# Optimization experiments

Measured on AMD Instinct MI355X. Metric: run time of the kernel, lower is better.

The kernel has to match this reference:

```python
import jax, jax.numpy as jnp
import numpy as np

B, S = 1, 2048
HID, NH, NKV, HD = 2048, 16, 4, 128
NREP = NH // NKV  # 4
WIN = 1024
ROPE_THETA = 10000.0


def rotate_half(t):
    t1, t2 = jnp.split(t, 2, axis=-1)
    return jnp.concatenate([-t2, t1], axis=-1)


def setup_inputs() -> dict:
    key = jax.random.key(0)
    ks = jax.random.split(key, 5)
    x = jax.random.normal(ks[0], (B, S, HID), dtype=jnp.float32)
    # causal sliding-window additive mask: 0 where attended, -1e9 elsewhere
    i = jnp.arange(S)
    allowed = (i[None, :] <= i[:, None]) & (i[:, None] - i[None, :] < WIN)
    attention_mask = jnp.where(allowed, 0.0, -1e9).astype(jnp.float32)[None, None]  # [1,1,S,S]
    wq = jax.random.normal(ks[1], (NH * HD, HID), dtype=jnp.float32) * 0.02
    wk = jax.random.normal(ks[2], (NKV * HD, HID), dtype=jnp.float32) * 0.02
    wv = jax.random.normal(ks[3], (NKV * HD, HID), dtype=jnp.float32) * 0.02
    wo = jax.random.normal(ks[4], (HID, NH * HD), dtype=jnp.float32) * 0.02
    return {"x": x, "attention_mask": attention_mask, "wq": wq, "wk": wk, "wv": wv, "wo": wo}


def reference(x, attention_mask, wq, wk, wv, wo):
    b, s, _ = x.shape
    q = (x @ wq.T).reshape(b, s, NH, HD)
    k = (x @ wk.T).reshape(b, s, NKV, HD)
    v = (x @ wv.T).reshape(b, s, NKV, HD)
    # rotary embeddings (HF-style rotate_half)
    inv_freq = 1.0 / (ROPE_THETA ** (jnp.arange(0, HD, 2, dtype=jnp.float32) / HD))
    freqs = jnp.arange(s, dtype=jnp.float32)[:, None] * inv_freq[None, :]  # [s, HD/2]
    emb = jnp.concatenate([freqs, freqs], axis=-1)  # [s, HD]
    cos = jnp.cos(emb)[None, :, None, :]
    sin = jnp.sin(emb)[None, :, None, :]
    q = q * cos + rotate_half(q) * sin
    k = k * cos + rotate_half(k) * sin
    # GQA: repeat kv heads
    k = jnp.repeat(k, NREP, axis=2)  # [b, s, NH, HD]
    v = jnp.repeat(v, NREP, axis=2)
    scores = jnp.einsum('bqhd,bkhd->bhqk', q, k) / jnp.sqrt(jnp.float32(HD)) + attention_mask
    probs = jax.nn.softmax(scores.astype(jnp.float32), axis=-1).astype(q.dtype)
    out = jnp.einsum('bhqk,bkhd->bqhd', probs, v).reshape(b, s, NH * HD)
    return out @ wo.T
```

## Files before the change

kernel.cpp:

```cpp
#include <hip/hip_runtime.h>


#define AS1 __attribute__((address_space(1)))
#define AS3 __attribute__((address_space(3)))

typedef short v8s __attribute__((ext_vector_type(8)));
typedef short v4s __attribute__((ext_vector_type(4)));
typedef float v4f __attribute__((ext_vector_type(4)));

__device__ __forceinline__ void gload16(const void* g, void* l) {
  __builtin_amdgcn_global_load_lds((AS1 void*)g, (AS3 void*)l, 16, 0, 0);
}

__device__ __forceinline__ short f2bf(float f) {
  union { float f; unsigned u; } v; v.f = f;
  unsigned r = (v.u + 0x7FFFu + ((v.u >> 16) & 1u)) >> 16;
  return (short)r;
}
__device__ __forceinline__ short f2bf_hu(float f) {
  union { float f; unsigned u; } v; v.f = f;
  return (short)((v.u + 0x8000u) >> 16);
}
__device__ __forceinline__ float bf2f(short h) {
  union { unsigned u; float f; } v; v.u = ((unsigned)(unsigned short)h) << 16;
  return v.f;
}
__device__ __forceinline__ bool sniff_bf16(const unsigned* mask) {
  return mask[1] == 0xCE6ECE6Eu;
}

__device__ __forceinline__ int colmap(int w, int nt, int r) {
  return (w & 1) * 32 + (nt & 1) * 16 + (nt >> 1) * 64 + r;
}

#define ROPE_L2T (13.287712379549449f / 64.0f)
#define Q_SCALE  (1.4426950408889634f * 0.08838834764831845f)
#define SM_SHIFT 8.0f

template <bool BF> struct Raw8;
template <> struct Raw8<true>  { v8s v; };
template <> struct Raw8<false> { float4 a, b; };

template <bool BF> __device__ __forceinline__ Raw8<BF> ldraw(const void* p, size_t e);
template <> __device__ __forceinline__ Raw8<true> ldraw<true>(const void* p, size_t e) {
  Raw8<true> r; r.v = *(const v8s*)((const short*)p + e); return r;
}
template <> __device__ __forceinline__ Raw8<false> ldraw<false>(const void* p, size_t e) {
  Raw8<false> r; const float* f = (const float*)p + e;
  r.a = *(const float4*)f; r.b = *(const float4*)(f + 4); return r;
}
template <bool BF> __device__ __forceinline__ v8s cvt8(const Raw8<BF>& r);
template <> __device__ __forceinline__ v8s cvt8<true>(const Raw8<true>& r) { return r.v; }
template <> __device__ __forceinline__ v8s cvt8<false>(const Raw8<false>& r) {
  v8s o;
  o[0] = f2bf(r.a.x); o[1] = f2bf(r.a.y); o[2] = f2bf(r.a.z); o[3] = f2bf(r.a.w);
  o[4] = f2bf(r.b.x); o[5] = f2bf(r.b.y); o[6] = f2bf(r.b.z); o[7] = f2bf(r.b.w);
  return o;
}

__global__ __launch_bounds__(256) void convert_kernel(
    const void* __restrict__ X, const void* __restrict__ WQ,
    const void* __restrict__ WK, const void* __restrict__ WV,
    const void* __restrict__ WO, const unsigned* __restrict__ mask,
    short* __restrict__ Xbf, short* __restrict__ Wqkvbf, short* __restrict__ WObf)
{
  const bool bf = sniff_bf16(mask);
  size_t e = ((size_t)blockIdx.x * 256 + threadIdx.x) * 8;
  const void* src; short* dst; size_t off, doff;
  if (e < 4194304)       { src = X;  dst = Xbf;  off = e; doff = e; }
  else if (e < 10485760) {
    size_t wv = e - 4194304; dst = Wqkvbf; doff = wv;
    if (wv < 4194304)      { src = WQ; off = wv; }
    else if (wv < 5242880) { src = WK; off = wv - 4194304; }
    else                   { src = WV; off = wv - 5242880; }
  }
  else                   { src = WO; dst = WObf; off = e - 10485760; doff = off; }
  v8s v = bf ? ldraw<true>(src, off).v : cvt8<false>(ldraw<false>(src, off));
  *(v8s*)&dst[doff] = v;
}

#define MM(I, J) acc##I##J = __builtin_amdgcn_mfma_f32_16x16x32_bf16(a##I, b##J, acc##I##J, 0, 0, 0)

#define GEMM128_BODY(Aptr, Bptr) \
  const int tid = threadIdx.x; \
  const int w = tid >> 6, lane = tid & 63; \
  const int quad = lane >> 4, r = lane & 15; \
  const int wm = (w >> 1) * 64; \
  const int rlo = lane >> 2, c8 = (lane & 3) * 8; \
  size_t ga[4]; short* la[4]; size_t gb[4]; short* lb[4]; \
  _Pragma("unroll") for (int j = 0; j < 4; ++j) { \
    int cc = w * 4 + j; int p = cc >> 3, local = cc & 7; \
    ga[j] = (size_t)(m0 + local * 16 + rlo) * 2048 + p * 32 + c8; \
    la[j] = lA + cc * 512; \
    gb[j] = (size_t)(n0 + local * 16 + rlo) * 2048 + p * 32 + c8; \
    lb[j] = lB + cc * 512; } \
  v4f acc00 = v4f{0.f, 0.f, 0.f, 0.f}; \
  v4f acc01 = acc00, acc02 = acc00, acc03 = acc00; \
  v4f acc10 = acc00, acc11 = acc00, acc12 = acc00, acc13 = acc00; \
  v4f acc20 = acc00, acc21 = acc00, acc22 = acc00, acc23 = acc00; \
  v4f acc30 = acc00, acc31 = acc00, acc32 = acc00, acc33 = acc00; \
  for (int k0 = 0; k0 < 2048; k0 += 64) { \
    if (k0) __syncthreads(); \
    _Pragma("unroll") for (int j = 0; j < 4; ++j) gload16(Aptr + ga[j] + k0, la[j]); \
    _Pragma("unroll") for (int j = 0; j < 4; ++j) gload16(Bptr + gb[j] + k0, lb[j]); \
    __syncthreads(); \
    _Pragma("unroll") for (int ks = 0; ks < 2; ++ks) { \
      const int ab = ks * 4096; \
      v8s a0 = *(const v8s*)&lA[ab + (wm +  0 + r) * 32 + quad * 8]; \
      v8s a1 = *(const v8s*)&lA[ab + (wm + 16 + r) * 32 + quad * 8]; \
      v8s a2 = *(const v8s*)&lA[ab + (wm + 32 + r) * 32 + quad * 8]; \
      v8s a3 = *(const v8s*)&lA[ab + (wm + 48 + r) * 32 + quad * 8]; \
      v8s b0 = *(const v8s*)&lB[ab + colmap(w, 0, r) * 32 + quad * 8]; \
      v8s b1 = *(const v8s*)&lB[ab + colmap(w, 1, r) * 32 + quad * 8]; \
      v8s b2 = *(const v8s*)&lB[ab + colmap(w, 2, r) * 32 + quad * 8]; \
      v8s b3 = *(const v8s*)&lB[ab + colmap(w, 3, r) * 32 + quad * 8]; \
      MM(0,0); MM(0,1); MM(0,2); MM(0,3); \
      MM(1,0); MM(1,1); MM(1,2); MM(1,3); \
      MM(2,0); MM(2,1); MM(2,2); MM(2,3); \
      MM(3,0); MM(3,1); MM(3,2); MM(3,3); \
    } \
  }

__global__ __launch_bounds__(256, 2) void gemm_qkv_dma(
    const short* __restrict__ Xbf, const short* __restrict__ Wqkvbf,
    short* __restrict__ Qo, short* __restrict__ Ko, short* __restrict__ VTo)
{
  __shared__ __align__(16) short lA[128 * 64];
  __shared__ __align__(16) short lB[128 * 64];
  const int m0 = blockIdx.x * 128;
  const int n0 = blockIdx.y * 128;
  GEMM128_BODY(Xbf, Wqkvbf)

  const int rowb = m0 + wm + quad * 4;
  if (n0 < 2560) {
    const bool isQ = (n0 < 2048);
    short* dst = isQ ? Qo : Ko;
    const int ld = isQ ? 2048 : 512;
    const int base = isQ ? n0 : (n0 - 2048);
    const float sc = isQ ? Q_SCALE : 1.0f;
#define ROPE_ST(MT, NT, X1, X2) { \
      int d = (w & 1) * 32 + NT * 16 + r; \
      float inv = exp2f(-(float)d * ROPE_L2T); \
      _Pragma("unroll") for (int i = 0; i < 4; ++i) { \
        int row = rowb + MT * 16 + i; \
        float ang = (float)row * inv; \
        float cs = cosf(ang), sn = sinf(ang); \
        float x1 = X1[i], x2 = X2[i]; \
        dst[(size_t)row * ld + base + d]      = f2bf((x1 * cs - x2 * sn) * sc); \
        dst[(size_t)row * ld + base + d + 64] = f2bf((x2 * cs + x1 * sn) * sc); } }
    ROPE_ST(0, 0, acc00, acc02) ROPE_ST(0, 1, acc01, acc03)
    ROPE_ST(1, 0, acc10, acc12) ROPE_ST(1, 1, acc11, acc13)
    ROPE_ST(2, 0, acc20, acc22) ROPE_ST(2, 1, acc21, acc23)
    ROPE_ST(3, 0, acc30, acc32) ROPE_ST(3, 1, acc31, acc33)
#undef ROPE_ST
  } else {
#define VT_ST(MT, NT, A) { \
      int row = rowb + MT * 16; \
      int vcol = n0 - 2560 + colmap(w, NT, r); \
      v4s pk; \
      _Pragma("unroll") for (int i = 0; i < 4; ++i) pk[i] = f2bf(A[i]); \
      *(v4s*)&VTo[(size_t)vcol * 2048 + row] = pk; }
    VT_ST(0, 0, acc00) VT_ST(0, 1, acc01) VT_ST(0, 2, acc02) VT_ST(0, 3, acc03)
    VT_ST(1, 0, acc10) VT_ST(1, 1, acc11) VT_ST(1, 2, acc12) VT_ST(1, 3, acc13)
    VT_ST(2, 0, acc20) VT_ST(2, 1, acc21) VT_ST(2, 2, acc22) VT_ST(2, 3, acc23)
    VT_ST(3, 0, acc30) VT_ST(3, 1, acc31) VT_ST(3, 2, acc32) VT_ST(3, 3, acc33)
#undef VT_ST
  }
}

__global__ __launch_bounds__(256, 2) void gemm_out_dma(
    const short* __restrict__ A, const short* __restrict__ WObf,
    const unsigned* __restrict__ mask, void* __restrict__ Out)
{
  __shared__ __align__(16) short lA[128 * 64];
  __shared__ __align__(16) short lB[128 * 64];
  const int m0 = blockIdx.x * 128;
  const int n0 = blockIdx.y * 128;
  GEMM128_BODY(A, WObf)

  const bool bf = sniff_bf16(mask);
  const int rowb = m0 + wm + quad * 4;
#define OUT_ST(MT, NT, ACC) { \
    int row = rowb + MT * 16; \
    int col = n0 + colmap(w, NT, r); \
    _Pragma("unroll") for (int i = 0; i < 4; ++i) { \
      size_t idx = (size_t)(row + i) * 2048 + col; \
      if (bf) ((short*)Out)[idx] = f2bf(ACC[i]); \
      else    ((float*)Out)[idx] = ACC[i]; } }
  OUT_ST(0, 0, acc00) OUT_ST(0, 1, acc01) OUT_ST(0, 2, acc02) OUT_ST(0, 3, acc03)
  OUT_ST(1, 0, acc10) OUT_ST(1, 1, acc11) OUT_ST(1, 2, acc12) OUT_ST(1, 3, acc13)
  OUT_ST(2, 0, acc20) OUT_ST(2, 1, acc21) OUT_ST(2, 2, acc22) OUT_ST(2, 3, acc23)
  OUT_ST(3, 0, acc30) OUT_ST(3, 1, acc31) OUT_ST(3, 2, acc32) OUT_ST(3, 3, acc33)
#undef OUT_ST
}

template <bool BFA, bool BFB>
__device__ __forceinline__ void gemm64x128_loop(
    const void* __restrict__ A, const void* __restrict__ Bt,
    int m0, int brow0, short* lA, short* lB, v4f acc[2][4])
{
  const int tid = threadIdx.x;
  const int w = tid >> 6, lane = tid & 63;
  const int quad = lane >> 4, r = lane & 15;
  const int wm = (w >> 1) * 32;

  int uoffA[2]; size_t ea[2];
#pragma unroll
  for (int j = 0; j < 2; ++j) {
    int u = tid + 256 * j;
    int row = u >> 3, c = (u & 7) * 8;
    uoffA[j] = (c & 32) * 64 + row * 32 + (c & 31);
    ea[j] = (size_t)(m0 + row) * 2048 + c;
  }
  int uoffB[4]; size_t eb[4];
#pragma unroll
  for (int j = 0; j < 4; ++j) {
    int u = tid + 256 * j;
    int row = u >> 3, c = (u & 7) * 8;
    uoffB[j] = (c & 32) * 128 + row * 32 + (c & 31);
    eb[j] = (size_t)(brow0 + row) * 2048 + c;
  }

  for (int k0 = 0; k0 < 2048; k0 += 64) {
    Raw8<BFA> ta[2]; Raw8<BFB> tb[4];
#pragma unroll
    for (int j = 0; j < 2; ++j) ta[j] = ldraw<BFA>(A, ea[j] + k0);
#pragma unroll
    for (int j = 0; j < 4; ++j) tb[j] = ldraw<BFB>(Bt, eb[j] + k0);
    if (k0) __syncthreads();
#pragma unroll
    for (int j = 0; j < 2; ++j) *(v8s*)&lA[uoffA[j]] = cvt8<BFA>(ta[j]);
#pragma unroll
    for (int j = 0; j < 4; ++j) *(v8s*)&lB[uoffB[j]] = cvt8<BFB>(tb[j]);
    __syncthreads();
#pragma unroll
    for (int ks = 0; ks < 2; ++ks) {
      v8s a[2], b[4];
#pragma unroll
      for (int mt = 0; mt < 2; ++mt)
        a[mt] = *(const v8s*)&lA[ks * 2048 + (wm + mt * 16 + r) * 32 + quad * 8];
#pragma unroll
      for (int nt = 0; nt < 4; ++nt)
        b[nt] = *(const v8s*)&lB[ks * 4096 + colmap(w, nt, r) * 32 + quad * 8];
#pragma unroll
      for (int mt = 0; mt < 2; ++mt)
#pragma unroll
        for (int nt = 0; nt < 4; ++nt)
          acc[mt][nt] = __builtin_amdgcn_mfma_f32_16x16x32_bf16(a[mt], b[nt], acc[mt][nt], 0, 0, 0);
    }
  }
}

__device__ __forceinline__ void qkv_epilogue_fb(
    v4f acc[2][4], int m0, int n0, short* Qo, short* Ko, short* VTo)
{
  const int tid = threadIdx.x;
  const int w = tid >> 6, lane = tid & 63;
  const int quad = lane >> 4, r = lane & 15;
  const int wm = (w >> 1) * 32;
  const int rowb = m0 + wm + quad * 4;

  if (n0 < 2560) {
    const bool isQ = (n0 < 2048);
    short* dst = isQ ? Qo : Ko;
    const int ld = isQ ? 2048 : 512;
    const int base = isQ ? n0 : (n0 - 2048);
    const float sc = isQ ? Q_SCALE : 1.0f;
#pragma unroll
    for (int nt = 0; nt < 2; ++nt) {
      int d = (w & 1) * 32 + nt * 16 + r;
      float inv = exp2f(-(float)d * ROPE_L2T);
#pragma unroll
      for (int mt = 0; mt < 2; ++mt)
#pragma unroll
        for (int i = 0; i < 4; ++i) {
          int row = rowb + mt * 16 + i;
          float ang = (float)row * inv;
          float cs = cosf(ang), sn = sinf(ang);
          float x1 = acc[mt][nt][i], x2 = acc[mt][nt + 2][i];
          dst[(size_t)row * ld + base + d]      = f2bf((x1 * cs - x2 * sn) * sc);
          dst[(size_t)row * ld + base + d + 64] = f2bf((x2 * cs + x1 * sn) * sc);
        }
    }
  } else {
#pragma unroll
    for (int mt = 0; mt < 2; ++mt)
#pragma unroll
      for (int nt = 0; nt < 4; ++nt) {
        int row = rowb + mt * 16;
        int vcol = n0 - 2560 + colmap(w, nt, r);
        v4s pk;
#pragma unroll
        for (int i = 0; i < 4; ++i) pk[i] = f2bf(acc[mt][nt][i]);
        *(v4s*)&VTo[(size_t)vcol * 2048 + row] = pk;
      }
  }
}

__global__ __launch_bounds__(256, 3) void gemm_qkv_fb(
    const void* __restrict__ X, const void* __restrict__ WQ,
    const void* __restrict__ WK, const void* __restrict__ WV,
    const unsigned* __restrict__ mask,
    short* __restrict__ Qo, short* __restrict__ Ko, short* __restrict__ VTo)
{
  __shared__ __align__(16) short lA[64 * 64];
  __shared__ __align__(16) short lB[128 * 64];
  const int m0 = blockIdx.x * 64;
  const int n0 = blockIdx.y * 128;
  const void* Bt; int brow0;
  if (n0 < 2048)      { Bt = WQ; brow0 = n0; }
  else if (n0 < 2560) { Bt = WK; brow0 = n0 - 2048; }
  else                { Bt = WV; brow0 = n0 - 2560; }

  v4f acc[2][4];
#pragma unroll
  for (int i = 0; i < 2; ++i)
#pragma unroll
    for (int j = 0; j < 4; ++j) acc[i][j] = v4f{0.f, 0.f, 0.f, 0.f};

  if (sniff_bf16(mask)) gemm64x128_loop<true, true>(X, Bt, m0, brow0, lA, lB, acc);
  else                  gemm64x128_loop<false, false>(X, Bt, m0, brow0, lA, lB, acc);
  qkv_epilogue_fb(acc, m0, n0, Qo, Ko, VTo);
}

__global__ __launch_bounds__(256, 3) void gemm_out_fb(
    const short* __restrict__ A, const void* __restrict__ WO,
    const unsigned* __restrict__ mask, void* __restrict__ Out)
{
  __shared__ __align__(16) short lA[64 * 64];
  __shared__ __align__(16) short lB[128 * 64];
  const bool bf = sniff_bf16(mask);
  const int m0 = blockIdx.x * 64;
  const int n0 = blockIdx.y * 128;

  v4f acc[2][4];
#pragma unroll
  for (int i = 0; i < 2; ++i)
#pragma unroll
    for (int j = 0; j < 4; ++j) acc[i][j] = v4f{0.f, 0.f, 0.f, 0.f};

  if (bf) gemm64x128_loop<true, true>(A, WO, m0, n0, lA, lB, acc);
  else    gemm64x128_loop<true, false>(A, WO, m0, n0, lA, lB, acc);

  const int tid = threadIdx.x;
  const int w = tid >> 6, lane = tid & 63;
  const int quad = lane >> 4, r = lane & 15;
  const int wm = (w >> 1) * 32;
  const int rowb = m0 + wm + quad * 4;
#pragma unroll
  for (int mt = 0; mt < 2; ++mt)
#pragma unroll
    for (int nt = 0; nt < 4; ++nt) {
      int row = rowb + mt * 16;
      int col = n0 + colmap(w, nt, r);
#pragma unroll
      for (int i = 0; i < 4; ++i) {
        size_t idx = (size_t)(row + i) * 2048 + col;
        if (bf) ((short*)Out)[idx] = f2bf(acc[mt][nt][i]);
        else    ((float*)Out)[idx] = acc[mt][nt][i];
      }
    }
}

__global__ __launch_bounds__(256, 1) void attn_kernel(
    const short* __restrict__ Q, const short* __restrict__ Kb,
    const short* __restrict__ VT, short* __restrict__ Ao)
{
  __shared__ __align__(16) short lK[64 * 128];
  __shared__ __align__(16) short lV[128 * 64];
  __shared__ __align__(16) short lP[4][16 * 72];

  const int bx = blockIdx.x;
  const int qb = bx >> 4, h = bx & 15;
  const int hk = h >> 2;
  const int q0 = qb * 64;
  const int tid = threadIdx.x, w = tid >> 6, lane = tid & 63;
  const int quad = lane >> 4, r = lane & 15;
  const int wq0 = q0 + w * 16;
  short* lPw = lP[w];

  v8s qa[4];
#pragma unroll
  for (int ks = 0; ks < 4; ++ks)
    qa[ks] = *(const v8s*)(Q + (size_t)(wq0 + r) * 2048 + h * 128 + ks * 32 + quad * 8);

  v8s ones;
#pragma unroll
  for (int j = 0; j < 8; ++j) ones[j] = (short)0x3F80;

  v4f Oa[8];
#pragma unroll
  for (int dt = 0; dt < 8; ++dt) Oa[dt] = v4f{0.f, 0.f, 0.f, 0.f};
  v4f La = v4f{0.f, 0.f, 0.f, 0.f};

  const int t0 = (q0 >= 1024) ? ((q0 - 1023) >> 6) : 0;
  const int t1 = qb;

  for (int t = t0; t <= t1; ++t) {
    const int key0 = t << 6;
    v8s tK[4], tV[4];
#pragma unroll
    for (int u = 0; u < 4; ++u) {
      int lin = (w * 4 + u) * 64 + lane;
      int krow = lin >> 4, kcc = lin & 15;
      tK[u] = *(const v8s*)(Kb + (size_t)(key0 + krow) * 512 + hk * 128 + ((kcc ^ krow) & 15) * 8);
      int vrow = lin >> 3, vcc = lin & 7;
      tV[u] = *(const v8s*)(VT + (size_t)(hk * 128 + vrow) * 2048 + key0 + ((vcc ^ vrow) & 7) * 8);
    }
    if (t > t0) __syncthreads();
#pragma unroll
    for (int u = 0; u < 4; ++u) {
      int lin = (w * 4 + u) * 64 + lane;
      *(v8s*)&lK[lin * 8] = tK[u];
      *(v8s*)&lV[lin * 8] = tV[u];
    }
    __syncthreads();

    v4f s4[4];
#pragma unroll
    for (int nt = 0; nt < 4; ++nt) s4[nt] = v4f{0.f, 0.f, 0.f, 0.f};
    __builtin_amdgcn_s_setprio(1);
#pragma unroll
    for (int ks = 0; ks < 4; ++ks)
#pragma unroll
      for (int nt = 0; nt < 4; ++nt) {
        v8s bk = *(const v8s*)&lK[(nt * 16 + r) * 128 + (((ks * 4 + quad) ^ r) & 15) * 8];
        s4[nt] = __builtin_amdgcn_mfma_f32_16x16x32_bf16(qa[ks], bk, s4[nt], 0, 0, 0);
      }
    __builtin_amdgcn_s_setprio(0);

    const bool full = (key0 + 63 <= wq0) && (wq0 + 15 - key0 < 1024);

    if (full) {
#pragma unroll
      for (int nt = 0; nt < 4; ++nt)
#pragma unroll
        for (int i = 0; i < 4; ++i)
          lPw[(quad * 4 + i) * 72 + nt * 16 + r] = f2bf_hu(exp2f(s4[nt][i] - SM_SHIFT));
    } else {
#pragma unroll
      for (int nt = 0; nt < 4; ++nt) {
        int d0 = wq0 + quad * 4 - key0 - nt * 16 - r;
#pragma unroll
        for (int i = 0; i < 4; ++i) {
          bool ok = (unsigned)(d0 + i) < 1024u;
          lPw[(quad * 4 + i) * 72 + nt * 16 + r] =
              ok ? f2bf_hu(exp2f(s4[nt][i] - SM_SHIFT)) : (short)0;
        }
      }
    }

    __builtin_amdgcn_s_setprio(1);
#pragma unroll
    for (int ks2 = 0; ks2 < 2; ++ks2) {
      v8s ap = *(const v8s*)&lPw[r * 72 + ks2 * 32 + quad * 8];
      La = __builtin_amdgcn_mfma_f32_16x16x32_bf16(ap, ones, La, 0, 0, 0);
#pragma unroll
      for (int dt = 0; dt < 8; ++dt) {
        v8s bv = *(const v8s*)&lV[(dt * 16 + r) * 64 + (((ks2 * 4 + quad) ^ r) & 7) * 8];
        Oa[dt] = __builtin_amdgcn_mfma_f32_16x16x32_bf16(ap, bv, Oa[dt], 0, 0, 0);
      }
    }
    __builtin_amdgcn_s_setprio(0);
  }

  float invl[4];
#pragma unroll
  for (int i = 0; i < 4; ++i) invl[i] = (La[i] > 0.f) ? 1.0f / La[i] : 0.f;
#pragma unroll
  for (int dt = 0; dt < 8; ++dt)
#pragma unroll
    for (int i = 0; i < 4; ++i) {
      int q = wq0 + quad * 4 + i;
      Ao[(size_t)q * 2048 + h * 128 + dt * 16 + r] = f2bf(Oa[dt][i] * invl[i]);
    }
}

extern "C" void kernel_launch(void* const* d_in, const int* in_sizes, int n_in,
                              void* d_out, int out_size, void* d_ws, size_t ws_size,
                              hipStream_t stream) {
  const void*     x    = d_in[0];
  const unsigned* mask = (const unsigned*)d_in[1];
  const void*     wq   = d_in[2];
  const void*     wk   = d_in[3];
  const void*     wv   = d_in[4];
  const void*     wo   = d_in[5];

  short* Q  = (short*)d_out;
  short* Kb = (short*)d_ws;
  short* VT = Kb + (size_t)1048576;
  short* Ao = VT + (size_t)1048576;

  const size_t NEED = 41943040ull;
  if (ws_size >= NEED) {
    short* Xbf    = Ao + (size_t)4194304;
    short* Wqkvbf = Xbf + (size_t)4194304;
    short* WObf   = Wqkvbf + (size_t)6291456;
    convert_kernel<<<7168, 256, 0, stream>>>(x, wq, wk, wv, wo, mask, Xbf, Wqkvbf, WObf);
    gemm_qkv_dma<<<dim3(16, 24), 256, 0, stream>>>(Xbf, Wqkvbf, Q, Kb, VT);
    attn_kernel<<<512, 256, 0, stream>>>(Q, Kb, VT, Ao);
    gemm_out_dma<<<dim3(16, 16), 256, 0, stream>>>(Ao, WObf, mask, d_out);
  } else {
    gemm_qkv_fb<<<dim3(32, 24), 256, 0, stream>>>(x, wq, wk, wv, mask, Q, Kb, VT);
    attn_kernel<<<512, 256, 0, stream>>>(Q, Kb, VT, Ao);
    gemm_out_fb<<<dim3(32, 16), 256, 0, stream>>>(Ao, wo, mask, d_out);
  }
}
```

Measured before the change: 235.3 us.

## Double-buffer LDS tiles in QKV and output projection GEMMs

Replaces the single-buffered K loop in both projection GEMMs with a double-buffered pipeline. The next 64-wide K tile is DMA-loaded into the alternate LDS buffer while the current tile is computed, using vmcnt waits and raw s_barrier instead of two __syncthreads per step. This is meant to hide global-load latency behind MFMA work. It doubles LDS per block to 64KB, which may limit occupancy to fewer blocks per CU.

```diff
diff --git a/kernel.cpp b/kernel.cpp
--- a/kernel.cpp
+++ b/kernel.cpp
@@ -81,55 +81,72 @@
 
 #define MM(I, J) acc##I##J = __builtin_amdgcn_mfma_f32_16x16x32_bf16(a##I, b##J, acc##I##J, 0, 0, 0)
 
-#define GEMM128_BODY(Aptr, Bptr) \
+#define STAGE8(Aptr, Bptr, K0, DA, DB) \
+    _Pragma("unroll") for (int j = 0; j < 4; ++j) gload16(Aptr + ga[j] + (K0), DA + la[j]); \
+    _Pragma("unroll") for (int j = 0; j < 4; ++j) gload16(Bptr + gb[j] + (K0), DB + lb[j]);
+
+#define COMPUTE64(SA, SB) \
+    _Pragma("unroll") for (int ks = 0; ks < 2; ++ks) { \
+      const int ab = ks * 4096; \
+      v8s a0 = *(const v8s*)&SA[ab + (wm +  0 + r) * 32 + quad * 8]; \
+      v8s a1 = *(const v8s*)&SA[ab + (wm + 16 + r) * 32 + quad * 8]; \
+      v8s a2 = *(const v8s*)&SA[ab + (wm + 32 + r) * 32 + quad * 8]; \
+      v8s a3 = *(const v8s*)&SA[ab + (wm + 48 + r) * 32 + quad * 8]; \
+      v8s b0 = *(const v8s*)&SB[ab + colmap(w, 0, r) * 32 + quad * 8]; \
+      v8s b1 = *(const v8s*)&SB[ab + colmap(w, 1, r) * 32 + quad * 8]; \
+      v8s b2 = *(const v8s*)&SB[ab + colmap(w, 2, r) * 32 + quad * 8]; \
+      v8s b3 = *(const v8s*)&SB[ab + colmap(w, 3, r) * 32 + quad * 8]; \
+      MM(0,0); MM(0,1); MM(0,2); MM(0,3); \
+      MM(1,0); MM(1,1); MM(1,2); MM(1,3); \
+      MM(2,0); MM(2,1); MM(2,2); MM(2,3); \
+      MM(3,0); MM(3,1); MM(3,2); MM(3,3); \
+    }
+
+#define GEMM128_DBUF_BODY(Aptr, Bptr) \
   const int tid = threadIdx.x; \
   const int w = tid >> 6, lane = tid & 63; \
   const int quad = lane >> 4, r = lane & 15; \
   const int wm = (w >> 1) * 64; \
   const int rlo = lane >> 2, c8 = (lane & 3) * 8; \
-  size_t ga[4]; short* la[4]; size_t gb[4]; short* lb[4]; \
+  size_t ga[4], gb[4]; int la[4], lb[4]; \
   _Pragma("unroll") for (int j = 0; j < 4; ++j) { \
     int cc = w * 4 + j; int p = cc >> 3, local = cc & 7; \
     ga[j] = (size_t)(m0 + local * 16 + rlo) * 2048 + p * 32 + c8; \
-    la[j] = lA + cc * 512; \
     gb[j] = (size_t)(n0 + local * 16 + rlo) * 2048 + p * 32 + c8; \
-    lb[j] = lB + cc * 512; } \
+    la[j] = cc * 512; lb[j] = cc * 512; } \
   v4f acc00 = v4f{0.f, 0.f, 0.f, 0.f}; \
   v4f acc01 = acc00, acc02 = acc00, acc03 = acc00; \
   v4f acc10 = acc00, acc11 = acc00, acc12 = acc00, acc13 = acc00; \
   v4f acc20 = acc00, acc21 = acc00, acc22 = acc00, acc23 = acc00; \
   v4f acc30 = acc00, acc31 = acc00, acc32 = acc00, acc33 = acc00; \
-  for (int k0 = 0; k0 < 2048; k0 += 64) { \
-    if (k0) __syncthreads(); \
-    _Pragma("unroll") for (int j = 0; j < 4; ++j) gload16(Aptr + ga[j] + k0, la[j]); \
-    _Pragma("unroll") for (int j = 0; j < 4; ++j) gload16(Bptr + gb[j] + k0, lb[j]); \
-    __syncthreads(); \
-    _Pragma("unroll") for (int ks = 0; ks < 2; ++ks) { \
-      const int ab = ks * 4096; \
-      v8s a0 = *(const v8s*)&lA[ab + (wm +  0 + r) * 32 + quad * 8]; \
-      v8s a1 = *(const v8s*)&lA[ab + (wm + 16 + r) * 32 + quad * 8]; \
-      v8s a2 = *(const v8s*)&lA[ab + (wm + 32 + r) * 32 + quad * 8]; \
-      v8s a3 = *(const v8s*)&lA[ab + (wm + 48 + r) * 32 + quad * 8]; \
-      v8s b0 = *(const v8s*)&lB[ab + colmap(w, 0, r) * 32 + quad * 8]; \
-      v8s b1 = *(const v8s*)&lB[ab + colmap(w, 1, r) * 32 + quad * 8]; \
-      v8s b2 = *(const v8s*)&lB[ab + colmap(w, 2, r) * 32 + quad * 8]; \
-      v8s b3 = *(const v8s*)&lB[ab + colmap(w, 3, r) * 32 + quad * 8]; \
-      MM(0,0); MM(0,1); MM(0,2); MM(0,3); \
-      MM(1,0); MM(1,1); MM(1,2); MM(1,3); \
-      MM(2,0); MM(2,1); MM(2,2); MM(2,3); \
-      MM(3,0); MM(3,1); MM(3,2); MM(3,3); \
-    } \
-  }
+  STAGE8(Aptr, Bptr, 0, lA0, lB0) \
+  for (int t = 0; t < 31; ++t) { \
+    const int k1 = (t + 1) * 64; \
+    short* sA = (t & 1) ? lA1 : lA0; short* sB = (t & 1) ? lB1 : lB0; \
+    short* dA = (t & 1) ? lA0 : lA1; short* dB = (t & 1) ? lB0 : lB1; \
+    STAGE8(Aptr, Bptr, k1, dA, dB) \
+    asm volatile("s_waitcnt vmcnt(8)" ::: "memory"); \
+    __builtin_amdgcn_sched_barrier(0); \
+    __builtin_amdgcn_s_barrier(); \
+    COMPUTE64(sA, sB) \
+    __builtin_amdgcn_s_barrier(); \
+  } \
+  asm volatile("s_waitcnt vmcnt(0)" ::: "memory"); \
+  __builtin_amdgcn_sched_barrier(0); \
+  __builtin_amdgcn_s_barrier(); \
+  COMPUTE64(lA1, lB1)
 
 __global__ __launch_bounds__(256, 2) void gemm_qkv_dma(
     const short* __restrict__ Xbf, const short* __restrict__ Wqkvbf,
     short* __restrict__ Qo, short* __restrict__ Ko, short* __restrict__ VTo)
 {
-  __shared__ __align__(16) short lA[128 * 64];
-  __shared__ __align__(16) short lB[128 * 64];
+  __shared__ __align__(16) short lA0[128 * 64];
+  __shared__ __align__(16) short lB0[128 * 64];
+  __shared__ __align__(16) short lA1[128 * 64];
+  __shared__ __align__(16) short lB1[128 * 64];
   const int m0 = blockIdx.x * 128;
   const int n0 = blockIdx.y * 128;
-  GEMM128_BODY(Xbf, Wqkvbf)
+  GEMM128_DBUF_BODY(Xbf, Wqkvbf)
 
   const int rowb = m0 + wm + quad * 4;
   if (n0 < 2560) {
@@ -172,11 +189,13 @@
     const short* __restrict__ A, const short* __restrict__ WObf,
     const unsigned* __restrict__ mask, void* __restrict__ Out)
 {
-  __shared__ __align__(16) short lA[128 * 64];
-  __shared__ __align__(16) short lB[128 * 64];
+  __shared__ __align__(16) short lA0[128 * 64];
+  __shared__ __align__(16) short lB0[128 * 64];
+  __shared__ __align__(16) short lA1[128 * 64];
+  __shared__ __align__(16) short lB1[128 * 64];
   const int m0 = blockIdx.x * 128;
   const int n0 = blockIdx.y * 128;
-  GEMM128_BODY(A, WObf)
+  GEMM128_DBUF_BODY(A, WObf)
 
   const bool bf = sniff_bf16(mask);
   const int rowb = m0 + wm + quad * 4;
```

New measurement: 232.3 us. No clear change (-1.3%).
